# Kernel optimization log

Measured on AMD Instinct MI355X. Metric: run time of the kernel, lower is better.

Reference implementation:

```python
import jax, jax.numpy as jnp
import numpy as np

EPS = 1e-5

def _conv1x1(x, w, b):
    # x: [B,C,...], w: [O,C], b: [O]
    y = jnp.einsum('oc,bc...->bo...', w, x)
    return y + b.reshape((1, -1) + (1,) * (x.ndim - 2))

def _bn(x, g, be, m, v):
    # inference-mode BatchNorm with running stats (PyTorch eps=1e-5)
    s = (1, -1) + (1,) * (x.ndim - 2)
    return (x - m.reshape(s)) * (g.reshape(s) / jnp.sqrt(v.reshape(s) + EPS)) + be.reshape(s)

def _patches3x3(x):
    # F.unfold(kernel=3, pad=1, stride=1, dil=1): [B,C,H,W] -> [B,C,9,H,W], row-major kernel order
    B, C, H, W = x.shape
    xp = jnp.pad(x, ((0, 0), (0, 0), (1, 1), (1, 1)))
    return jnp.stack([xp[:, :, ky:ky + H, kx:kx + W] for ky in range(3) for kx in range(3)], axis=2)

def setup_inputs() -> dict:
    key = jax.random.key(0)
    ks = jax.random.split(key, 40)
    B, Cin, H, W = 4, 16, 192, 192
    Cm = 64  # mlp[-1]
    d = {}
    d['x'] = jax.random.normal(ks[0], (B, Cin, H, W), jnp.float32)
    d['group_mask'] = jnp.ones((B, 1, H, W), jnp.float32)
    d['group_xyz'] = jax.random.normal(ks[1], (B, 3, 9, H, W), jnp.float32)
    def bnp(k, c):
        k1, k2, k3, k4 = jax.random.split(k, 4)
        return (1.0 + 0.1 * jax.random.normal(k1, (c,)), 0.1 * jax.random.normal(k2, (c,)),
                0.1 * jax.random.normal(k3, (c,)), 0.5 + jax.random.uniform(k4, (c,)))
    d['w0'] = 0.1 * jax.random.normal(ks[2], (Cm, Cin)); d['b0'] = 0.01 * jax.random.normal(ks[3], (Cm,))
    d['g0'], d['beta0'], d['m0'], d['v0'] = bnp(ks[4], Cm)
    wn_dims = [(8, 3), (8, 8), (16, 8)]
    for i, (o, c) in enumerate(wn_dims):
        d[f'wn_w{i}'] = 0.3 * jax.random.normal(ks[5 + 3 * i], (o, c))
        d[f'wn_b{i}'] = 0.01 * jax.random.normal(ks[6 + 3 * i], (o,))
        d[f'wn_g{i}'], d[f'wn_beta{i}'], d[f'wn_m{i}'], d[f'wn_v{i}'] = bnp(ks[7 + 3 * i], o)
    d['lw'] = 0.05 * jax.random.normal(ks[20], (Cm, 16 * Cm)); d['lb'] = 0.01 * jax.random.normal(ks[21], (Cm,))
    d['lg'], d['lbeta'], d['lm'], d['lv'] = bnp(ks[22], Cm)
    return d

def reference(x, group_mask, group_xyz,
              w0, b0, g0, beta0, m0, v0,
              wn_w0, wn_b0, wn_g0, wn_beta0, wn_m0, wn_v0,
              wn_w1, wn_b1, wn_g1, wn_beta1, wn_m1, wn_v1,
              wn_w2, wn_b2, wn_g2, wn_beta2, wn_m2, wn_v2,
              lw, lb, lg, lbeta, lm, lv):
    # mlp_convs chain (single layer here)
    x = jax.nn.relu(_bn(_conv1x1(x, w0, b0), g0, beta0, m0, v0))  # [B,Cm,H,W]
    B, _, N, H, W = group_xyz.shape
    # WeightNet on local coords: [B,3,N,H*W] -> [B,16,N,H*W]
    gz = group_xyz.reshape(B, 3, N, H * W)
    for w, b, g, be, m, v in ((wn_w0, wn_b0, wn_g0, wn_beta0, wn_m0, wn_v0),
                              (wn_w1, wn_b1, wn_g1, wn_beta1, wn_m1, wn_v1),
                              (wn_w2, wn_b2, wn_g2, wn_beta2, wn_m2, wn_v2)):
        gz = jax.nn.relu(_bn(_conv1x1(gz, w, b), g, be, m, v))
    gz = gz.reshape(B, 16, N, H, W)
    p = _patches3x3(x)  # [B,Cm,9,H,W]
    C = p.shape[1]
    # per-pixel matmul: [B,H,W,C,9] @ [B,H,W,9,16] -> [B,H,W,C,16]
    out = jnp.einsum('bckhw,bokhw->bhwco', p, gz)
    out = out.reshape(B, H, W, C * 16).transpose(0, 3, 1, 2)  # [B,16*Cm,H,W]
    return jax.nn.relu(_bn(_conv1x1(out, lw, lb), lg, lbeta, lm, lv))
```

## Files before the change

kernel.cpp:

```cpp
#include <hip/hip_runtime.h>
#include <hip/hip_bf16.h>

#define HH 192
#define WW 192
#define HWPROD (192*192)
#define EPSBN 1e-5f

typedef _Float16 f16x8 __attribute__((ext_vector_type(8)));
typedef _Float16 f16x4 __attribute__((ext_vector_type(4)));
typedef _Float16 f16x2 __attribute__((ext_vector_type(2)));
typedef float f32x4 __attribute__((ext_vector_type(4)));
typedef float f32x16 __attribute__((ext_vector_type(16)));

__global__ __launch_bounds__(256) void prep_conv0_k(
                       const float* __restrict__ w0, const float* __restrict__ b0,
                       const float* __restrict__ g0, const float* __restrict__ beta0,
                       const float* __restrict__ m0, const float* __restrict__ v0,
                       const float* __restrict__ wnw0, const float* __restrict__ wnb0,
                       const float* __restrict__ wng0, const float* __restrict__ wnbe0,
                       const float* __restrict__ wnm0, const float* __restrict__ wnv0,
                       const float* __restrict__ wnw1, const float* __restrict__ wnb1,
                       const float* __restrict__ wng1, const float* __restrict__ wnbe1,
                       const float* __restrict__ wnm1, const float* __restrict__ wnv1,
                       const float* __restrict__ wnw2, const float* __restrict__ wnb2,
                       const float* __restrict__ wng2, const float* __restrict__ wnbe2,
                       const float* __restrict__ wnm2, const float* __restrict__ wnv2,
                       const float* __restrict__ lw, const float* __restrict__ lb,
                       const float* __restrict__ lg, const float* __restrict__ lbeta,
                       const float* __restrict__ lm, const float* __restrict__ lv,
                       const float* __restrict__ x,
                       _Float16* __restrict__ x1L,
                       _Float16* __restrict__ whF,
                       float* __restrict__ lbf,
                       float* __restrict__ wnP)
{
    const int tid = threadIdx.x;

    if (blockIdx.x >= 576) {
        int idx = (blockIdx.x - 576) * 256 + tid;
        if (idx < 65536) {
            int j    = idx & 7;
            int lane = (idx >> 3) & 63;
            int kg   = (idx >> 9) & 63;
            int nt   = idx >> 15;
            int k = kg * 16 + ((lane >> 5) & 1) * 8 + j;
            int n = nt * 32 + (lane & 31);
            float s = lg[n] * rsqrtf(lv[n] + EPSBN);
            whF[idx] = (_Float16)(lw[n * 1024 + k] * s);
        } else if (idx < 65600) {
            int j = idx - 65536;
            float s = lg[j] * rsqrtf(lv[j] + EPSBN);
            lbf[j] = (lb[j] - lm[j]) * s + lbeta[j];
        } else if (idx < 65848) {
            int t = idx - 65600;
            if (t < 24)       { int o = t / 3;           float s = wng0[o] * rsqrtf(wnv0[o] + EPSBN); wnP[t] = wnw0[t] * s; }
            else if (t < 32)  { int o = t - 24;          float s = wng0[o] * rsqrtf(wnv0[o] + EPSBN); wnP[t] = (wnb0[o] - wnm0[o]) * s + wnbe0[o]; }
            else if (t < 96)  { int t2 = t - 32;  int o = t2 >> 3; float s = wng1[o] * rsqrtf(wnv1[o] + EPSBN); wnP[t] = wnw1[t2] * s; }
            else if (t < 104) { int o = t - 96;          float s = wng1[o] * rsqrtf(wnv1[o] + EPSBN); wnP[t] = (wnb1[o] - wnm1[o]) * s + wnbe1[o]; }
            else if (t < 232) { int t2 = t - 104; int o = t2 >> 3; float s = wng2[o] * rsqrtf(wnv2[o] + EPSBN); wnP[t] = wnw2[t2] * s; }
            else if (t < 248) { int o = t - 232;         float s = wng2[o] * rsqrtf(wnv2[o] + EPSBN); wnP[t] = (wnb2[o] - wnm2[o]) * s + wnbe2[o]; }
        }
        return;
    }

    __shared__ float wSt[16][64];
    __shared__ float bS[64];
    for (int t = tid; t < 1024; t += 256) {
        int o = t >> 4, ci = t & 15;
        float s = g0[o] * rsqrtf(v0[o] + EPSBN);
        wSt[ci][o] = w0[t] * s;
    }
    if (tid < 64) {
        float s = g0[tid] * rsqrtf(v0[tid] + EPSBN);
        bS[tid] = (b0[tid] - m0[tid]) * s + beta0[tid];
    }
    __syncthreads();

    const int pix = blockIdx.x * 256 + tid;
    const int b = pix / HWPROD;
    const int p = pix - b * HWPROD;

    float xv[16];
#pragma unroll
    for (int cin = 0; cin < 16; cin++)
        xv[cin] = x[((size_t)b * 16 + cin) * HWPROD + p];

    _Float16* outp = x1L + (size_t)pix * 64;
#pragma unroll
    for (int co = 0; co < 64; co += 4) {
        f32x4 a = { bS[co], bS[co + 1], bS[co + 2], bS[co + 3] };
#pragma unroll
        for (int cin = 0; cin < 16; cin++) {
            float xc = xv[cin];
            a.x += wSt[cin][co + 0] * xc;
            a.y += wSt[cin][co + 1] * xc;
            a.z += wSt[cin][co + 2] * xc;
            a.w += wSt[cin][co + 3] * xc;
        }
        a.x = fmaxf(a.x, 0.f); a.y = fmaxf(a.y, 0.f);
        a.z = fmaxf(a.z, 0.f); a.w = fmaxf(a.w, 0.f);
        *(f16x4*)(outp + co) = __builtin_convertvector(a, f16x4);
    }
}

__global__ __launch_bounds__(512, 4) void pconv_main_k(const float* __restrict__ gxyz,
                                                       const _Float16* __restrict__ x1L,
                                                       const _Float16* __restrict__ whF,
                                                       const float* __restrict__ lbf,
                                                       const float* __restrict__ wnP,
                                                       float* __restrict__ out)
{
    __shared__ __align__(16) char smem[58496];
    f16x2*    xtP = reinterpret_cast<f16x2*>(smem);
    _Float16* A0  = reinterpret_cast<_Float16*>(smem + 25728);
    _Float16* A1  = reinterpret_cast<_Float16*>(smem + 42112);
    _Float16* gzF = reinterpret_cast<_Float16*>(smem + 25728);
    float*    Cb  = reinterpret_cast<float*>(smem);
    float*    Pb  = reinterpret_cast<float*>(smem + 25728);

    const int tid = threadIdx.x;
    const int bid = blockIdx.x;
    const int b   = bid / (HH * 3);
    const int rem = bid % (HH * 3);
    const int h   = rem / 3;
    const int wc0 = (rem % 3) * 64;

    for (int q = tid; q < 1584; q += 512) {
        int c8   = q & 7;
        int colr = q >> 3;
        int col  = colr % 66;
        int r    = colr / 66;
        int hr = h + r - 1;
        int wc = wc0 + col - 1;
        union { f16x8 v; f16x2 p[4]; } U;
        U.v = f16x8{};
        if (hr >= 0 && hr < HH && wc >= 0 && wc < WW) {
            U.v = *(const f16x8*)(x1L + (((size_t)b * HH + hr) * WW + wc) * 64 + c8 * 8);
        }
#pragma unroll
        for (int i = 0; i < 4; i++)
            xtP[(c8 * 4 + i) * 201 + colr] = U.p[i];
    }

    for (int u = tid; u < 576; u += 512) {
        int pixu = u & 63, tap = u >> 6;
        size_t base = ((size_t)(b * 3) * 9 + tap) * HWPROD + (size_t)h * WW + wc0 + pixu;
        float z0 = gxyz[base];
        float z1 = gxyz[base + (size_t)9 * HWPROD];
        float z2 = gxyz[base + (size_t)18 * HWPROD];
        float h0[8], h1[8];
#pragma unroll
        for (int o = 0; o < 8; o++) {
            float a = wnP[24 + o] + wnP[o * 3 + 0] * z0 + wnP[o * 3 + 1] * z1 + wnP[o * 3 + 2] * z2;
            h0[o] = fmaxf(a, 0.f);
        }
#pragma unroll
        for (int o = 0; o < 8; o++) {
            float a = wnP[96 + o];
#pragma unroll
            for (int c = 0; c < 8; c++) a += wnP[32 + o * 8 + c] * h0[c];
            h1[o] = fmaxf(a, 0.f);
        }
        float g[16];
#pragma unroll
        for (int o = 0; o < 16; o++) {
            float a = wnP[232 + o];
#pragma unroll
            for (int c = 0; c < 8; c++) a += wnP[104 + o * 8 + c] * h1[c];
            g[o] = fmaxf(a, 0.f);
        }
        f16x8 lo, hi;
#pragma unroll
        for (int o = 0; o < 8; o++) { lo[o] = (_Float16)g[o]; hi[o] = (_Float16)g[o + 8]; }
        *(f16x8*)&gzF[pixu * 152 + tap * 16]     = lo;
        *(f16x8*)&gzF[pixu * 152 + tap * 16 + 8] = hi;
    }
    __syncthreads();

    const int pix = tid & 63;
    const int u8  = tid >> 6;
    const int oh  = u8 & 1;
    const int cp  = u8 >> 1;
    const int lane = tid & 63;
    const int wv   = tid >> 6;
    const int mt32w = wv & 1;
    const int nt32  = (wv >> 1) & 1;
    const int kh    = wv >> 2;

    f16x2 gq2[9][4];
#pragma unroll
    for (int t = 0; t < 9; t++) {
        union { f16x8 v; f16x2 h[4]; } G;
        G.v = *(const f16x8*)&gzF[pix * 152 + t * 16 + oh * 8];
#pragma unroll
        for (int d = 0; d < 4; d++) gq2[t][d] = G.h[d];
    }
    __syncthreads();

    const int mt32p = pix >> 5;
    const int p31   = pix & 31;

    auto phase1 = [&](int cc, _Float16* Ab) {
        union { f16x2 h2[4]; f16x8 v; } av0, av1;
#pragma unroll
        for (int d = 0; d < 4; d++) { av0.h2[d] = f16x2{0, 0}; av1.h2[d] = f16x2{0, 0}; }
        const f16x2* xrow = xtP + (cc * 4 + cp) * 201 + pix;
#pragma unroll
        for (int ky = 0; ky < 3; ky++) {
#pragma unroll
            for (int kx = 0; kx < 3; kx++) {
                const int t = ky * 3 + kx;
                f16x2 xq = xrow[ky * 66 + kx];
                f16x2 xb0 = __builtin_shufflevector(xq, xq, 0, 0);
                f16x2 xb1 = __builtin_shufflevector(xq, xq, 1, 1);
#pragma unroll
                for (int d = 0; d < 4; d++) {
                    av0.h2[d] = __builtin_elementwise_fma(xb0, gq2[t][d], av0.h2[d]);
                    av1.h2[d] = __builtin_elementwise_fma(xb1, gq2[t][d], av1.h2[d]);
                }
            }
        }
        const int u0 = (cp * 4 + mt32p) * 64 + oh * 32 + p31;
        *(f16x8*)&Ab[u0 * 8]         = av0.v;
        *(f16x8*)&Ab[(u0 + 128) * 8] = av1.v;
    };

    const f16x8* whF8 = (const f16x8*)whF;
    f32x16 facc;
#pragma unroll
    for (int r = 0; r < 16; r++) facc[r] = 0.f;

    phase1(0, A0);
    __syncthreads();

#pragma unroll 2
    for (int cc = 0; cc < 8; cc++) {
        const _Float16* Ac = (cc & 1) ? A1 : A0;
        if ((cc & 1) == kh) {
#pragma unroll
            for (int kgl = 0; kgl < 8; kgl++) {
                f16x8 a  = *(const f16x8*)&Ac[(((kgl * 2 + mt32w) * 64) + lane) * 8];
                f16x8 wh = whF8[(nt32 * 64 + cc * 8 + kgl) * 64 + lane];
                facc = __builtin_amdgcn_mfma_f32_32x32x16_f16(a, wh, facc, 0, 0, 0);
            }
        }
        if (cc < 7) phase1(cc + 1, (cc & 1) ? A0 : A1);
        __syncthreads();
    }

    const int tile = mt32w * 2 + nt32;
    if (kh == 1) {
#pragma unroll
        for (int r = 0; r < 16; r++)
            Pb[(tile * 16 + r) * 64 + lane] = facc[r];
    }
    __syncthreads();
    if (kh == 0) {
        const int n = nt32 * 32 + (lane & 31);
        const float bias = lbf[n];
        const int rbase = mt32w * 32 + 4 * (lane >> 5);
#pragma unroll
        for (int r = 0; r < 16; r++) {
            float vsum = facc[r] + Pb[(tile * 16 + r) * 64 + lane] + bias;
            const int pixm = rbase + (r & 3) + 8 * (r >> 2);
            Cb[n * 67 + pixm] = fmaxf(vsum, 0.f);
        }
    }
    __syncthreads();
    {
        const int pixq = tid & 63, jq = tid >> 6;
        size_t ob = ((size_t)b * 64 + jq * 8) * HWPROD + (size_t)h * WW + wc0 + pixq;
#pragma unroll
        for (int i = 0; i < 8; i++) {
            out[ob + (size_t)i * HWPROD] = Cb[(jq * 8 + i) * 67 + pixq];
        }
    }
}

extern "C" void kernel_launch(void* const* d_in, const int* in_sizes, int n_in,
                              void* d_out, int out_size, void* d_ws, size_t ws_size,
                              hipStream_t stream) {
    const float* x    = (const float*)d_in[0];
    const float* gxyz = (const float*)d_in[2];

    char* ws = (char*)d_ws;
    _Float16* x1L = (_Float16*)ws;
    _Float16* whF = x1L + 9437184;
    float* lbf = (float*)(whF + 65536);
    float* wnP = lbf + 64;

    prep_conv0_k<<<838, 256, 0, stream>>>(
        (const float*)d_in[3],  (const float*)d_in[4],  (const float*)d_in[5],
        (const float*)d_in[6],  (const float*)d_in[7],  (const float*)d_in[8],
        (const float*)d_in[9],  (const float*)d_in[10], (const float*)d_in[11],
        (const float*)d_in[12], (const float*)d_in[13], (const float*)d_in[14],
        (const float*)d_in[15], (const float*)d_in[16], (const float*)d_in[17],
        (const float*)d_in[18], (const float*)d_in[19], (const float*)d_in[20],
        (const float*)d_in[21], (const float*)d_in[22], (const float*)d_in[23],
        (const float*)d_in[24], (const float*)d_in[25], (const float*)d_in[26],
        (const float*)d_in[27], (const float*)d_in[28], (const float*)d_in[29],
        (const float*)d_in[30], (const float*)d_in[31], (const float*)d_in[32],
        x, x1L, whF, lbf, wnP);

    pconv_main_k<<<4 * HH * 3, 512, 0, stream>>>(gxyz, x1L, whF, lbf, wnP,
                                                 (float*)d_out);
}
```

Measured before the change: 225.2 us.

## Restructure pointconv main kernel into 128-thread 2x32 tiles with register-fed MFMA

The main kernel now uses 128-thread blocks, each covering two rows by 32 columns. Each wave computes the per-pixel patch×weight products in registers and feeds them straight into MFMA, instead of staging them through double-buffered shared-memory A tiles with a split-K reduction across waves. Shared memory drops from about 58 KB to about 19 KB, and most intra-loop barriers go away. Inline-asm packed FMAs with op_sel replace the explicit broadcast shuffles. In exchange, each wave reloads the linear-layer weights from global memory for every channel pair, and the smaller blocks give less latency hiding per block.

```diff
diff --git a/kernel.cpp b/kernel.cpp
--- a/kernel.cpp
+++ b/kernel.cpp
@@ -103,48 +103,30 @@
     }
 }
 
-__global__ __launch_bounds__(512, 4) void pconv_main_k(const float* __restrict__ gxyz,
+__global__ __launch_bounds__(128, 4) void pconv_main_k(const float* __restrict__ gxyz,
                                                        const _Float16* __restrict__ x1L,
                                                        const _Float16* __restrict__ whF,
                                                        const float* __restrict__ lbf,
                                                        const float* __restrict__ wnP,
                                                        float* __restrict__ out)
 {
-    __shared__ __align__(16) char smem[58496];
-    f16x2*    xtP = reinterpret_cast<f16x2*>(smem);
-    _Float16* A0  = reinterpret_cast<_Float16*>(smem + 25728);
-    _Float16* A1  = reinterpret_cast<_Float16*>(smem + 42112);
-    _Float16* gzF = reinterpret_cast<_Float16*>(smem + 25728);
-    float*    Cb  = reinterpret_cast<float*>(smem);
-    float*    Pb  = reinterpret_cast<float*>(smem + 25728);
+    __shared__ __align__(16) char smem[19456];
+    unsigned*  xSu = reinterpret_cast<unsigned*>(smem);
+    _Float16*  gzF = reinterpret_cast<_Float16*>(smem);
+    float*     Cb  = reinterpret_cast<float*>(smem);
 
     const int tid = threadIdx.x;
     const int bid = blockIdx.x;
-    const int b   = bid / (HH * 3);
-    const int rem = bid % (HH * 3);
-    const int h   = rem / 3;
-    const int wc0 = (rem % 3) * 64;
-
-    for (int q = tid; q < 1584; q += 512) {
-        int c8   = q & 7;
-        int colr = q >> 3;
-        int col  = colr % 66;
-        int r    = colr / 66;
-        int hr = h + r - 1;
-        int wc = wc0 + col - 1;
-        union { f16x8 v; f16x2 p[4]; } U;
-        U.v = f16x8{};
-        if (hr >= 0 && hr < HH && wc >= 0 && wc < WW) {
-            U.v = *(const f16x8*)(x1L + (((size_t)b * HH + hr) * WW + wc) * 64 + c8 * 8);
-        }
-#pragma unroll
-        for (int i = 0; i < 4; i++)
-            xtP[(c8 * 4 + i) * 201 + colr] = U.p[i];
-    }
-
-    for (int u = tid; u < 576; u += 512) {
-        int pixu = u & 63, tap = u >> 6;
-        size_t base = ((size_t)(b * 3) * 9 + tap) * HWPROD + (size_t)h * WW + wc0 + pixu;
+    const int b   = bid / (96 * 6);
+    const int rem = bid % (96 * 6);
+    const int hb  = rem / 6;
+    const int c6  = rem % 6;
+    const int h   = hb * 2;
+    const int wc0 = c6 * 32;
+
+    for (int u = tid; u < 576; u += 128) {
+        int col = u & 31, rrow = (u >> 5) & 1, tap = u >> 6;
+        size_t base = ((size_t)(b * 3) * 9 + tap) * HWPROD + (size_t)(h + rrow) * WW + wc0 + col;
         float z0 = gxyz[base];
         float z1 = gxyz[base + (size_t)9 * HWPROD];
         float z2 = gxyz[base + (size_t)18 * HWPROD];
@@ -172,107 +154,118 @@
         f16x8 lo, hi;
 #pragma unroll
         for (int o = 0; o < 8; o++) { lo[o] = (_Float16)g[o]; hi[o] = (_Float16)g[o + 8]; }
-        *(f16x8*)&gzF[pixu * 152 + tap * 16]     = lo;
-        *(f16x8*)&gzF[pixu * 152 + tap * 16 + 8] = hi;
-    }
-    __syncthreads();
-
-    const int pix = tid & 63;
-    const int u8  = tid >> 6;
-    const int oh  = u8 & 1;
-    const int cp  = u8 >> 1;
+        int pixb = u & 63;
+        *(f16x8*)&gzF[pixb * 152 + tap * 16]     = lo;
+        *(f16x8*)&gzF[pixb * 152 + tap * 16 + 8] = hi;
+    }
+    __syncthreads();
+
     const int lane = tid & 63;
-    const int wv   = tid >> 6;
-    const int mt32w = wv & 1;
-    const int nt32  = (wv >> 1) & 1;
-    const int kh    = wv >> 2;
+    const int w    = tid >> 6;
+    const int p31  = lane & 31;
+    const int oh   = lane >> 5;
+    const int pixb = w * 32 + p31;
 
     f16x2 gq2[9][4];
 #pragma unroll
     for (int t = 0; t < 9; t++) {
         union { f16x8 v; f16x2 h[4]; } G;
-        G.v = *(const f16x8*)&gzF[pix * 152 + t * 16 + oh * 8];
+        G.v = *(const f16x8*)&gzF[pixb * 152 + t * 16 + oh * 8];
 #pragma unroll
         for (int d = 0; d < 4; d++) gq2[t][d] = G.h[d];
     }
     __syncthreads();
 
-    const int mt32p = pix >> 5;
-    const int p31   = pix & 31;
-
-    auto phase1 = [&](int cc, _Float16* Ab) {
+    for (int i = 0; i < 16; i++) {
+        int u  = i * 128 + tid;
+        int cq = u & 15;
+        int cc = ((u >> 4) & 31) + 1;
+        int rr = u >> 9;
+        int hr = h + rr - 1;
+        uint2 v = {0u, 0u};
+        if (hr >= 0 && hr < HH)
+            v = *(const uint2*)(x1L + (((size_t)b * HH + hr) * WW + wc0 + cc - 1) * 64 + cq * 4);
+        xSu[(2 * cq) * 137 + rr * 34 + cc]     = v.x;
+        xSu[(2 * cq + 1) * 137 + rr * 34 + cc] = v.y;
+    }
+    {
+        int cq   = tid & 15;
+        int side = (tid >> 4) & 1;
+        int rr   = tid >> 5;
+        int cc   = side ? 33 : 0;
+        int hr = h + rr - 1;
+        int wc = wc0 + cc - 1;
+        uint2 v = {0u, 0u};
+        if (hr >= 0 && hr < HH && wc >= 0 && wc < WW)
+            v = *(const uint2*)(x1L + (((size_t)b * HH + hr) * WW + wc) * 64 + cq * 4);
+        xSu[(2 * cq) * 137 + rr * 34 + cc]     = v.x;
+        xSu[(2 * cq + 1) * 137 + rr * 34 + cc] = v.y;
+    }
+    __syncthreads();
+
+    const f16x8* whF8 = (const f16x8*)whF;
+    const unsigned* xrow = xSu + w * 34 + p31;
+
+    f32x16 facc0, facc1;
+#pragma unroll
+    for (int r = 0; r < 16; r++) { facc0[r] = 0.f; facc1[r] = 0.f; }
+
+#pragma unroll 2
+    for (int cb = 0; cb < 32; cb++) {
+        const int c0 = 2 * cb, c1 = 2 * cb + 1;
+        const f16x8 wh00 = whF8[(0 * 64 + c0) * 64 + lane];
+        const f16x8 wh01 = whF8[(1 * 64 + c0) * 64 + lane];
+        const f16x8 wh10 = whF8[(0 * 64 + c1) * 64 + lane];
+        const f16x8 wh11 = whF8[(1 * 64 + c1) * 64 + lane];
+
         union { f16x2 h2[4]; f16x8 v; } av0, av1;
 #pragma unroll
         for (int d = 0; d < 4; d++) { av0.h2[d] = f16x2{0, 0}; av1.h2[d] = f16x2{0, 0}; }
-        const f16x2* xrow = xtP + (cc * 4 + cp) * 201 + pix;
+        const unsigned* xr = xrow + cb * 137;
 #pragma unroll
         for (int ky = 0; ky < 3; ky++) {
 #pragma unroll
             for (int kx = 0; kx < 3; kx++) {
                 const int t = ky * 3 + kx;
-                f16x2 xq = xrow[ky * 66 + kx];
-                f16x2 xb0 = __builtin_shufflevector(xq, xq, 0, 0);
-                f16x2 xb1 = __builtin_shufflevector(xq, xq, 1, 1);
+                f16x2 xq;
+                { unsigned tmp = xr[ky * 34 + kx]; xq = *(f16x2*)&tmp; }
 #pragma unroll
                 for (int d = 0; d < 4; d++) {
-                    av0.h2[d] = __builtin_elementwise_fma(xb0, gq2[t][d], av0.h2[d]);
-                    av1.h2[d] = __builtin_elementwise_fma(xb1, gq2[t][d], av1.h2[d]);
+                    asm("v_pk_fma_f16 %0, %1, %2, %0 op_sel:[0,0,0] op_sel_hi:[0,1,1]"
+                        : "+v"(av0.h2[d]) : "v"(xq), "v"(gq2[t][d]));
+                    asm("v_pk_fma_f16 %0, %1, %2, %0 op_sel:[1,0,0] op_sel_hi:[1,1,1]"
+                        : "+v"(av1.h2[d]) : "v"(xq), "v"(gq2[t][d]));
                 }
             }
         }
-        const int u0 = (cp * 4 + mt32p) * 64 + oh * 32 + p31;
-        *(f16x8*)&Ab[u0 * 8]         = av0.v;
-        *(f16x8*)&Ab[(u0 + 128) * 8] = av1.v;
-    };
-
-    const f16x8* whF8 = (const f16x8*)whF;
-    f32x16 facc;
-#pragma unroll
-    for (int r = 0; r < 16; r++) facc[r] = 0.f;
-
-    phase1(0, A0);
-    __syncthreads();
-
-#pragma unroll 2
-    for (int cc = 0; cc < 8; cc++) {
-        const _Float16* Ac = (cc & 1) ? A1 : A0;
-        if ((cc & 1) == kh) {
-#pragma unroll
-            for (int kgl = 0; kgl < 8; kgl++) {
-                f16x8 a  = *(const f16x8*)&Ac[(((kgl * 2 + mt32w) * 64) + lane) * 8];
-                f16x8 wh = whF8[(nt32 * 64 + cc * 8 + kgl) * 64 + lane];
-                facc = __builtin_amdgcn_mfma_f32_32x32x16_f16(a, wh, facc, 0, 0, 0);
-            }
-        }
-        if (cc < 7) phase1(cc + 1, (cc & 1) ? A0 : A1);
-        __syncthreads();
-    }
-
-    const int tile = mt32w * 2 + nt32;
-    if (kh == 1) {
-#pragma unroll
-        for (int r = 0; r < 16; r++)
-            Pb[(tile * 16 + r) * 64 + lane] = facc[r];
-    }
-    __syncthreads();
-    if (kh == 0) {
-        const int n = nt32 * 32 + (lane & 31);
-        const float bias = lbf[n];
-        const int rbase = mt32w * 32 + 4 * (lane >> 5);
+        facc0 = __builtin_amdgcn_mfma_f32_32x32x16_f16(av0.v, wh00, facc0, 0, 0, 0);
+        facc1 = __builtin_amdgcn_mfma_f32_32x32x16_f16(av0.v, wh01, facc1, 0, 0, 0);
+        facc0 = __builtin_amdgcn_mfma_f32_32x32x16_f16(av1.v, wh10, facc0, 0, 0, 0);
+        facc1 = __builtin_amdgcn_mfma_f32_32x32x16_f16(av1.v, wh11, facc1, 0, 0, 0);
+    }
+    __syncthreads();
+
+    {
+        const int n0 = p31;
+        const float bias0 = lbf[n0];
+        const float bias1 = lbf[n0 + 32];
 #pragma unroll
         for (int r = 0; r < 16; r++) {
-            float vsum = facc[r] + Pb[(tile * 16 + r) * 64 + lane] + bias;
-            const int pixm = rbase + (r & 3) + 8 * (r >> 2);
-            Cb[n * 67 + pixm] = fmaxf(vsum, 0.f);
+            const int m = (r & 3) + 8 * (r >> 2) + 4 * oh;
+            Cb[n0 * 67 + w * 32 + m]        = fmaxf(facc0[r] + bias0, 0.f);
+            Cb[(n0 + 32) * 67 + w * 32 + m] = fmaxf(facc1[r] + bias1, 0.f);
         }
     }
     __syncthreads();
     {
-        const int pixq = tid & 63, jq = tid >> 6;
-        size_t ob = ((size_t)b * 64 + jq * 8) * HWPROD + (size_t)h * WW + wc0 + pixq;
-#pragma unroll
-        for (int i = 0; i < 8; i++) {
-            out[ob + (size_t)i * HWPROD] = Cb[(jq * 8 + i) * 67 + pixq];
+        const int col = tid & 31;
+        const int nq  = tid >> 5;
+#pragma unroll
+        for (int rr = 0; rr < 2; rr++) {
+            size_t ob = ((size_t)b * 64 + nq * 16) * HWPROD + (size_t)(h + rr) * WW + wc0 + col;
+#pragma unroll
+            for (int i = 0; i < 16; i++)
+                out[ob + (size_t)i * HWPROD] = Cb[(nq * 16 + i) * 67 + rr * 32 + col];
         }
     }
 }
@@ -302,6 +295,6 @@
         (const float*)d_in[30], (const float*)d_in[31], (const float*)d_in[32],
         x, x1L, whF, lbf, wnP);
 
-    pconv_main_k<<<4 * HH * 3, 512, 0, stream>>>(gxyz, x1L, whF, lbf, wnP,
+    pconv_main_k<<<4 * 96 * 6, 128, 0, stream>>>(gxyz, x1L, whF, lbf, wnP,
                                                  (float*)d_out);
 }
```

New measurement: 215.1 us. -4.5%, faster.
